# Kernel tuning notes

Hardware: AMD Instinct MI355X
Metric: run time of the kernel (lower is better)

The kernel has to match this reference:

```python
import jax, jax.numpy as jnp
import numpy as np

EMBED_DIM = 1024
NUM_HEADS = 16
HEAD_DIM = EMBED_DIM // NUM_HEADS
L, B, S = 2048, 2, 2048


def setup_inputs() -> dict:
    key = jax.random.key(0)
    k1, k2, k3, k4, k5, k6, k7 = jax.random.split(key, 7)
    query = jax.random.normal(k1, (L, B, EMBED_DIM), dtype=jnp.float32)
    kk = jax.random.normal(k2, (S, B, EMBED_DIM), dtype=jnp.float32)
    vv = jax.random.normal(k3, (S, B, EMBED_DIM), dtype=jnp.float32)
    # in_proj: Linear(E, 3E) -> weight (3E, E), bias (3E,)
    w_in = jax.random.normal(k4, (3 * EMBED_DIM, EMBED_DIM), dtype=jnp.float32) * (1.0 / np.sqrt(EMBED_DIM))
    b_in = jax.random.normal(k5, (3 * EMBED_DIM,), dtype=jnp.float32) * 0.02
    w_out = jax.random.normal(k6, (EMBED_DIM, EMBED_DIM), dtype=jnp.float32) * (1.0 / np.sqrt(EMBED_DIM))
    b_out = jax.random.normal(k7, (EMBED_DIM,), dtype=jnp.float32) * 0.02
    return {"query": query, "key": kk, "value": vv,
            "w_in": w_in, "b_in": b_in, "w_out": w_out, "b_out": b_out}


def _split_heads(x, seq_len, batch):
    # (T, B, E) -> (B, H, T, d)
    return x.reshape(seq_len, batch, NUM_HEADS, HEAD_DIM).transpose(1, 2, 0, 3)


def reference(query, key, value, w_in, b_in, w_out, b_out):
    seq_q, batch, _ = query.shape
    seq_kv = key.shape[0]
    # split fused in_proj into q/k/v projections (chunk along output rows)
    wq, wk, wv = jnp.split(w_in, 3, axis=0)
    bq, bk, bv = jnp.split(b_in, 3, axis=0)
    q = query @ wq.T + bq            # (L, B, E)
    k = key @ wk.T + bk              # (S, B, E)
    v = value @ wv.T + bv            # (S, B, E)
    q = _split_heads(q, seq_q, batch)   # (B, H, L, d)
    k = _split_heads(k, seq_kv, batch)  # (B, H, S, d)
    v = _split_heads(v, seq_kv, batch)  # (B, H, S, d)
    scale = jnp.asarray(np.sqrt(HEAD_DIM), dtype=q.dtype)
    scores = jnp.einsum('bhld,bhsd->bhls', q, k) / scale  # (B, H, L, S)
    attn = jax.nn.softmax(scores, axis=-1)
    context = jnp.einsum('bhls,bhsd->bhld', attn, v)      # (B, H, L, d)
    # (B, H, L, d) -> (L, B, E)
    context = context.transpose(2, 0, 1, 3).reshape(seq_q, batch, EMBED_DIM)
    attn_output = context @ w_out.T + b_out
    return attn_output
```

## Files before the change

### kernel.cpp

```cpp
#include <hip/hip_runtime.h>
#include <hip/hip_bf16.h>
#include <stdint.h>

#define L_SEQ 2048
#define S_SEQ 2048
#define BATCH 2
#define EMB 1024
#define NH 16
#define HD 64
#define MROWS 4096

typedef __bf16 bf16x8 __attribute__((ext_vector_type(8)));
typedef float f32x4 __attribute__((ext_vector_type(4)));
typedef __hip_bfloat16 bf16;

__device__ __forceinline__ f32x4 mfma16(bf16x8 a, bf16x8 b, f32x4 c) {
    return __builtin_amdgcn_mfma_f32_16x16x32_bf16(a, b, c, 0, 0, 0);
}

__device__ __forceinline__ void gll16(const bf16* g, bf16* l) {
    __builtin_amdgcn_global_load_lds(
        (const __attribute__((address_space(1))) void*)g,
        (__attribute__((address_space(3))) void*)l, 16, 0, 0);
}

__device__ __forceinline__ bf16x8 ld8_cvt(const float* p) {
    const float4 a = *reinterpret_cast<const float4*>(p);
    const float4 b = *reinterpret_cast<const float4*>(p + 4);
    union { bf16x8 v; bf16 h[8]; } u;
    u.h[0] = __float2bfloat16(a.x); u.h[1] = __float2bfloat16(a.y);
    u.h[2] = __float2bfloat16(a.z); u.h[3] = __float2bfloat16(a.w);
    u.h[4] = __float2bfloat16(b.x); u.h[5] = __float2bfloat16(b.y);
    u.h[6] = __float2bfloat16(b.z); u.h[7] = __float2bfloat16(b.w);
    return u.v;
}

__device__ __forceinline__ uint32_t packbf2(float a, float b) {
    const uint32_t ra = __float_as_uint(a) + 0x8000u;
    const uint32_t rb = __float_as_uint(b) + 0x8000u;
    return __builtin_amdgcn_perm(rb, ra, 0x07060302u);
}

__device__ __forceinline__ bf16x8 pfrag(const uint32_t* pk0, const uint32_t* pk1, int sk) {
    auto t0 = __builtin_amdgcn_permlane32_swap(pk0[2 * sk], pk0[2 * sk + 1], false, false);
    auto a02 = __builtin_amdgcn_permlane16_swap(t0[0], t0[1], false, false);
    auto t1 = __builtin_amdgcn_permlane32_swap(pk1[2 * sk], pk1[2 * sk + 1], false, false);
    auto a13 = __builtin_amdgcn_permlane16_swap(t1[0], t1[1], false, false);
    union { uint32_t u[4]; bf16x8 v; } pf;
    pf.u[0] = a02[0]; pf.u[1] = a13[0]; pf.u[2] = a02[1]; pf.u[3] = a13[1];
    return pf.v;
}

__global__ __launch_bounds__(256) void cvt_kernel(
    const float* __restrict__ w_in, const float* __restrict__ w_out,
    const float* __restrict__ q_in, const float* __restrict__ k_in,
    const float* __restrict__ v_in,
    bf16* __restrict__ wib, bf16* __restrict__ wob,
    bf16* __restrict__ Xq, bf16* __restrict__ Xk, bf16* __restrict__ Xv)
{
    const size_t i = ((size_t)blockIdx.x * 256 + threadIdx.x) * 8;
    const size_t o1 = (size_t)3 * EMB * EMB;
    const size_t o2 = o1 + (size_t)EMB * EMB;
    const size_t o3 = o2 + (size_t)MROWS * EMB;
    const size_t o4 = o3 + (size_t)MROWS * EMB;
    const float* src; bf16* dst; size_t j;
    if      (i < o1) { src = w_in;  dst = wib; j = i; }
    else if (i < o2) { src = w_out; dst = wob; j = i - o1; }
    else if (i < o3) { src = q_in;  dst = Xq;  j = i - o2; }
    else if (i < o4) { src = k_in;  dst = Xk;  j = i - o3; }
    else             { src = v_in;  dst = Xv;  j = i - o4; }
    *reinterpret_cast<bf16x8*>(dst + j) = ld8_cvt(src + j);
}

__global__ __launch_bounds__(256) void qkv_gemm(
    const bf16* __restrict__ Xq, const bf16* __restrict__ Xk,
    const bf16* __restrict__ Xv, const bf16* __restrict__ wib,
    const float* __restrict__ b_in,
    bf16* __restrict__ Qh, bf16* __restrict__ Kh, bf16* __restrict__ Vt)
{
    __shared__ alignas(16) bf16 lds_a[2][128 * 32];
    __shared__ alignas(16) bf16 lds_b[2][128 * 32];

    const int tid  = threadIdx.x;
    const int lane = tid & 63;
    const int wv   = tid >> 6;
    const int quad = lane >> 4;
    const int lx   = lane & 15;

    const int m0  = blockIdx.x * 128;
    const int n0g = blockIdx.y * 128;
    const int chunk = n0g >> 10;
    const bf16* Aop = (chunk == 0) ? Xq : (chunk == 1) ? Xk : Xv;

    const int wm = (wv >> 1) * 64;
    const int wn = (wv & 1) * 64;

    const int gr = 16 * wv + (lane >> 2);
    const int gc = (lane & 3) * 8;
    const bf16* gA = Aop + (size_t)(m0 + gr) * EMB + gc;
    const bf16* gB = wib + (size_t)(n0g + gr) * EMB + gc;
    bf16* lA = &lds_a[0][wv * 512];
    bf16* lB = &lds_b[0][wv * 512];
    const int BUF = 128 * 32;

    f32x4 acc[4][4];
#pragma unroll
    for (int i = 0; i < 4; i++)
#pragma unroll
        for (int j = 0; j < 4; j++) acc[i][j] = (f32x4){0.f, 0.f, 0.f, 0.f};

    gll16(gA, lA);
    gll16(gA + 64 * EMB, lA + 2048);
    gll16(gB, lB);
    gll16(gB + 64 * EMB, lB + 2048);
    __syncthreads();

    int cur = 0;
    for (int kt = 0; kt < EMB; kt += 32) {
        if (kt + 32 < EMB) {
            const int nx = cur ^ 1;
            gll16(gA + kt + 32, lA + nx * BUF);
            gll16(gA + 64 * EMB + kt + 32, lA + nx * BUF + 2048);
            gll16(gB + kt + 32, lB + nx * BUF);
            gll16(gB + 64 * EMB + kt + 32, lB + nx * BUF + 2048);
        }

        bf16x8 af[4], bfv[4];
        const int ka = quad * 8;
        const bf16* pa = &lds_a[cur][0];
        const bf16* pb = &lds_b[cur][0];
#pragma unroll
        for (int sm = 0; sm < 4; sm++)
            af[sm] = *reinterpret_cast<const bf16x8*>(pa + (wm + sm * 16 + lx) * 32 + ka);
#pragma unroll
        for (int sn = 0; sn < 4; sn++)
            bfv[sn] = *reinterpret_cast<const bf16x8*>(pb + (wn + sn * 16 + lx) * 32 + ka);
#pragma unroll
        for (int sm = 0; sm < 4; sm++)
#pragma unroll
            for (int sn = 0; sn < 4; sn++)
                acc[sm][sn] = mfma16(af[sm], bfv[sn], acc[sm][sn]);

        if (kt + 32 < EMB) __syncthreads();
        cur ^= 1;
    }

    const float scale = (chunk == 0) ? 0.18033688011112042f : 1.0f;
    bf16* dst = (chunk == 0) ? Qh : (chunk == 1) ? Kh : Vt;
#pragma unroll
    for (int sn = 0; sn < 4; sn++) {
        const int n_g = n0g + wn + sn * 16 + lx;
        const float bias = b_in[n_g];
        const int nc = n_g & (EMB - 1);
        const int h  = nc >> 6;
        const int dd = nc & 63;
#pragma unroll
        for (int sm = 0; sm < 4; sm++) {
#pragma unroll
            for (int r = 0; r < 4; r++) {
                const int m_g = m0 + wm + sm * 16 + quad * 4 + r;
                const int t = m_g >> 1;
                const int b = m_g & 1;
                const int bhidx = b * NH + h;
                const float v = (acc[sm][sn][r] + bias) * scale;
                const size_t off = (chunk == 2)
                    ? ((size_t)bhidx * HD + dd) * S_SEQ + t
                    : ((size_t)bhidx * S_SEQ + t) * HD + dd;
                dst[off] = __float2bfloat16(v);
            }
        }
    }
}

__global__ __launch_bounds__(256, 2) void attn_kernel(
    const bf16* __restrict__ Qh, const bf16* __restrict__ Kh,
    const bf16* __restrict__ Vt, bf16* __restrict__ ctx)
{
    __shared__ alignas(16) bf16 k_lds[2][128 * 64];
    __shared__ alignas(16) bf16 v_lds[2][64 * 128];

    const int tid  = threadIdx.x;
    const int lane = tid & 63;
    const int wv   = tid >> 6;
    const int quad = lane >> 4;
    const int lx   = lane & 15;
    const int lx7  = lane & 7;

    const int bh = blockIdx.y;
    const int l0 = blockIdx.x * 128;
    const int q0 = wv * 32;

    const bf16* Kbase = Kh + (size_t)bh * S_SEQ * HD;
    const bf16* Vbase = Vt + (size_t)bh * HD * S_SEQ;

    const bf16* qrow = Qh + ((size_t)bh * L_SEQ + l0 + q0 + lx) * HD + quad * 8;
    const bf16x8 qa0 = *reinterpret_cast<const bf16x8*>(qrow);
    const bf16x8 qa1 = *reinterpret_cast<const bf16x8*>(qrow + 32);
    const bf16x8 qb0 = *reinterpret_cast<const bf16x8*>(qrow + 16 * HD);
    const bf16x8 qb1 = *reinterpret_cast<const bf16x8*>(qrow + 16 * HD + 32);

    f32x4 rva = (f32x4){0.f, 0.f, 0.f, 0.f};
    f32x4 rvb = (f32x4){0.f, 0.f, 0.f, 0.f};
    f32x4 acca[4], accb[4];
#pragma unroll
    for (int sn = 0; sn < 4; sn++) {
        acca[sn] = (f32x4){0.f, 0.f, 0.f, 0.f};
        accb[sn] = (f32x4){0.f, 0.f, 0.f, 0.f};
    }

    const int kr = tid >> 3;
    const int kj = tid & 7;
    const bf16* gK = Kbase + (size_t)kr * HD + ((kj ^ (kr & 7)) << 3);
    const int vd = tid >> 4;
    const int vj = tid & 15;
    const bf16* gV = Vbase + (size_t)vd * S_SEQ + ((vj ^ (vd & 7)) << 3);

    bf16* kdst[2] = { &k_lds[0][wv * 512], &k_lds[1][wv * 512] };
    bf16* vdst[2] = { &v_lds[0][wv * 512], &v_lds[1][wv * 512] };

#pragma unroll
    for (int i = 0; i < 4; i++) {
        gll16(gK + (size_t)(i * 32) * HD, kdst[0] + i * 2048);
        gll16(gV + (size_t)(i * 16) * S_SEQ, vdst[0] + i * 2048);
    }

    int cur = 0;
    for (int s0 = 0; s0 < S_SEQ; s0 += 128) {
        __syncthreads();

        if (s0 + 128 < S_SEQ) {
            bf16* kd = kdst[cur ^ 1];
            bf16* vdp = vdst[cur ^ 1];
#pragma unroll
            for (int i = 0; i < 4; i++) {
                gll16(gK + (size_t)(s0 + 128 + i * 32) * HD, kd + i * 2048);
                gll16(gV + (size_t)(i * 16) * S_SEQ + s0 + 128, vdp + i * 2048);
            }
        }
        const bf16* kb = &k_lds[cur][0];
        const bf16* vb = &v_lds[cur][0];

        f32x4 sa[8], sb[8];
#pragma unroll
        for (int c = 0; c < 8; c++) {
            const bf16* krp = kb + (c * 16 + lx) * 64;
            bf16x8 kf0 = *reinterpret_cast<const bf16x8*>(krp + ((quad ^ lx7) << 3));
            bf16x8 kf1 = *reinterpret_cast<const bf16x8*>(krp + (((quad + 4) ^ lx7) << 3));
            f32x4 t0 = (f32x4){0.f, 0.f, 0.f, 0.f};
            t0 = mfma16(kf0, qa0, t0);
            t0 = mfma16(kf1, qa1, t0);
            sa[c] = t0;
            f32x4 t1 = (f32x4){0.f, 0.f, 0.f, 0.f};
            t1 = mfma16(kf0, qb0, t1);
            t1 = mfma16(kf1, qb1, t1);
            sb[c] = t1;
        }

        uint32_t pka0[8], pka1[8], pkb0[8], pkb1[8];
#pragma unroll
        for (int c = 0; c < 8; c++) {
#pragma unroll
            for (int r = 0; r < 4; r++) sa[c][r] = __builtin_amdgcn_exp2f(sa[c][r]);
            rva += sa[c];
            pka0[c] = packbf2(sa[c][0], sa[c][1]);
            pka1[c] = packbf2(sa[c][2], sa[c][3]);
        }
#pragma unroll
        for (int c = 0; c < 8; c++) {
#pragma unroll
            for (int r = 0; r < 4; r++) sb[c][r] = __builtin_amdgcn_exp2f(sb[c][r]);
            rvb += sb[c];
            pkb0[c] = packbf2(sb[c][0], sb[c][1]);
            pkb1[c] = packbf2(sb[c][2], sb[c][3]);
        }

#pragma unroll
        for (int sk = 0; sk < 4; sk++) {
            const bf16x8 pfa = pfrag(pka0, pka1, sk);
            const bf16x8 pfb = pfrag(pkb0, pkb1, sk);
#pragma unroll
            for (int sn = 0; sn < 4; sn++) {
                const bf16x8 vf = *reinterpret_cast<const bf16x8*>(
                    vb + (sn * 16 + lx) * 128 + (((sk * 4 + quad) ^ lx7) << 3));
                acca[sn] = mfma16(pfa, vf, acca[sn]);
                accb[sn] = mfma16(pfb, vf, accb[sn]);
            }
        }
        cur ^= 1;
    }

    float la = (rva[0] + rva[1]) + (rva[2] + rva[3]);
    la += __shfl_xor(la, 16);
    la += __shfl_xor(la, 32);
    float lbs = (rvb[0] + rvb[1]) + (rvb[2] + rvb[3]);
    lbs += __shfl_xor(lbs, 16);
    lbs += __shfl_xor(lbs, 32);

    const int b = bh >> 4;
    const int h = bh & 15;
#pragma unroll
    for (int r = 0; r < 4; r++) {
        const float lra = __shfl(la, quad * 20 + r);
        const float lrb = __shfl(lbs, quad * 20 + r);
        const float inva = 1.f / lra;
        const float invb = 1.f / lrb;
        const int lA = l0 + q0 + quad * 4 + r;
        const int lB = lA + 16;
#pragma unroll
        for (int sn = 0; sn < 4; sn++) {
            const int dd = sn * 16 + lx;
            ctx[(size_t)(lA * BATCH + b) * EMB + h * HD + dd] =
                __float2bfloat16(acca[sn][r] * inva);
            ctx[(size_t)(lB * BATCH + b) * EMB + h * HD + dd] =
                __float2bfloat16(accb[sn][r] * invb);
        }
    }
}

__global__ __launch_bounds__(256) void out_gemm(
    const bf16* __restrict__ ctx, const bf16* __restrict__ wob,
    const float* __restrict__ b_out, float* __restrict__ out)
{
    __shared__ alignas(16) bf16 lds_a[2][64 * 32];
    __shared__ alignas(16) bf16 lds_b[2][128 * 32];

    const int tid  = threadIdx.x;
    const int lane = tid & 63;
    const int wv   = tid >> 6;
    const int quad = lane >> 4;
    const int lx   = lane & 15;

    const int m0 = blockIdx.x * 64;
    const int n0 = blockIdx.y * 128;

    const int wm = (wv >> 1) * 32;
    const int wn = (wv & 1) * 64;

    const int gr = 16 * wv + (lane >> 2);
    const int gc = (lane & 3) * 8;
    const bf16* gA = ctx + (size_t)(m0 + gr) * EMB + gc;
    const bf16* gB = wob + (size_t)(n0 + gr) * EMB + gc;
    bf16* lA = &lds_a[0][wv * 512];
    bf16* lB = &lds_b[0][wv * 512];
    const int BUFA = 64 * 32;
    const int BUFB = 128 * 32;

    f32x4 acc[2][4];
#pragma unroll
    for (int i = 0; i < 2; i++)
#pragma unroll
        for (int j = 0; j < 4; j++) acc[i][j] = (f32x4){0.f, 0.f, 0.f, 0.f};

    gll16(gA, lA);
    gll16(gB, lB);
    gll16(gB + 64 * EMB, lB + 2048);
    __syncthreads();

    int cur = 0;
    for (int kt = 0; kt < EMB; kt += 32) {
        if (kt + 32 < EMB) {
            const int nx = cur ^ 1;
            gll16(gA + kt + 32, lA + nx * BUFA);
            gll16(gB + kt + 32, lB + nx * BUFB);
            gll16(gB + 64 * EMB + kt + 32, lB + nx * BUFB + 2048);
        }

        bf16x8 af[2], bfv[4];
        const int ka = quad * 8;
        const bf16* pa = &lds_a[cur][0];
        const bf16* pb = &lds_b[cur][0];
#pragma unroll
        for (int sm = 0; sm < 2; sm++)
            af[sm] = *reinterpret_cast<const bf16x8*>(pa + (wm + sm * 16 + lx) * 32 + ka);
#pragma unroll
        for (int sn = 0; sn < 4; sn++)
            bfv[sn] = *reinterpret_cast<const bf16x8*>(pb + (wn + sn * 16 + lx) * 32 + ka);
#pragma unroll
        for (int sm = 0; sm < 2; sm++)
#pragma unroll
            for (int sn = 0; sn < 4; sn++)
                acc[sm][sn] = mfma16(af[sm], bfv[sn], acc[sm][sn]);

        if (kt + 32 < EMB) __syncthreads();
        cur ^= 1;
    }

#pragma unroll
    for (int sn = 0; sn < 4; sn++) {
        const int n_g = n0 + wn + sn * 16 + lx;
        const float bias = b_out[n_g];
#pragma unroll
        for (int sm = 0; sm < 2; sm++) {
#pragma unroll
            for (int r = 0; r < 4; r++) {
                const int m_g = m0 + wm + sm * 16 + quad * 4 + r;
                out[(size_t)m_g * EMB + n_g] = acc[sm][sn][r] + bias;
            }
        }
    }
}

extern "C" void kernel_launch(void* const* d_in, const int* in_sizes, int n_in,
                              void* d_out, int out_size, void* d_ws, size_t ws_size,
                              hipStream_t stream)
{
    const float* query = (const float*)d_in[0];
    const float* key_  = (const float*)d_in[1];
    const float* value = (const float*)d_in[2];
    const float* w_in  = (const float*)d_in[3];
    const float* b_in  = (const float*)d_in[4];
    const float* w_out = (const float*)d_in[5];
    const float* b_out = (const float*)d_in[6];
    float* out = (float*)d_out;

    const size_t seg = (size_t)MROWS * EMB;
    bf16* wib = (bf16*)d_ws;
    bf16* wob = wib + (size_t)3 * EMB * EMB;
    bf16* Xq  = wob + (size_t)EMB * EMB;
    bf16* Xk  = Xq + seg;
    bf16* Xv  = Xk + seg;
    bf16* Qh  = Xv + seg;
    bf16* Kh  = Qh + seg;
    bf16* Vt  = Kh + seg;
    bf16* ctx = Xq;

    cvt_kernel<<<8192, 256, 0, stream>>>(w_in, w_out, query, key_, value,
                                         wib, wob, Xq, Xk, Xv);
    qkv_gemm<<<dim3(32, 24), 256, 0, stream>>>(Xq, Xk, Xv, wib, b_in, Qh, Kh, Vt);
    attn_kernel<<<dim3(16, 32), 256, 0, stream>>>(Qh, Kh, Vt, ctx);
    out_gemm<<<dim3(64, 8), 256, 0, stream>>>(ctx, wob, b_out, out);
}
```

Baseline: 217.2 us.

## Fuse fp32-to-bf16 activation conversion into QKV GEMM tile loads

Removes the separate conversion of query/key/value to bf16 and instead streams fp32 activation tiles directly into LDS via global_load_lds with an XOR swizzle. Conversion to bf16 happens while building MFMA fragments. This drops a full read+write pass over 3x4096x1024 activations, but doubles the A-tile LDS footprint and global traffic per GEMM tile (each tile is re-read by 8 column blocks in fp32), and adds packing ALU work in the inner loop.

```diff
diff --git a/kernel.cpp b/kernel.cpp
--- a/kernel.cpp
+++ b/kernel.cpp
@@ -19,6 +19,11 @@
 }
 
 __device__ __forceinline__ void gll16(const bf16* g, bf16* l) {
+    __builtin_amdgcn_global_load_lds(
+        (const __attribute__((address_space(1))) void*)g,
+        (__attribute__((address_space(3))) void*)l, 16, 0, 0);
+}
+__device__ __forceinline__ void gllf(const float* g, float* l) {
     __builtin_amdgcn_global_load_lds(
         (const __attribute__((address_space(1))) void*)g,
         (__attribute__((address_space(3))) void*)l, 16, 0, 0);
@@ -41,6 +46,13 @@
     return __builtin_amdgcn_perm(rb, ra, 0x07060302u);
 }
 
+__device__ __forceinline__ bf16x8 pack8(float4 lo, float4 hi) {
+    union { uint32_t u[4]; bf16x8 v; } t;
+    t.u[0] = packbf2(lo.x, lo.y); t.u[1] = packbf2(lo.z, lo.w);
+    t.u[2] = packbf2(hi.x, hi.y); t.u[3] = packbf2(hi.z, hi.w);
+    return t.v;
+}
+
 __device__ __forceinline__ bf16x8 pfrag(const uint32_t* pk0, const uint32_t* pk1, int sk) {
     auto t0 = __builtin_amdgcn_permlane32_swap(pk0[2 * sk], pk0[2 * sk + 1], false, false);
     auto a02 = __builtin_amdgcn_permlane16_swap(t0[0], t0[1], false, false);
@@ -53,55 +65,45 @@
 
 __global__ __launch_bounds__(256) void cvt_kernel(
     const float* __restrict__ w_in, const float* __restrict__ w_out,
-    const float* __restrict__ q_in, const float* __restrict__ k_in,
-    const float* __restrict__ v_in,
-    bf16* __restrict__ wib, bf16* __restrict__ wob,
-    bf16* __restrict__ Xq, bf16* __restrict__ Xk, bf16* __restrict__ Xv)
+    bf16* __restrict__ wib, bf16* __restrict__ wob)
 {
     const size_t i = ((size_t)blockIdx.x * 256 + threadIdx.x) * 8;
     const size_t o1 = (size_t)3 * EMB * EMB;
-    const size_t o2 = o1 + (size_t)EMB * EMB;
-    const size_t o3 = o2 + (size_t)MROWS * EMB;
-    const size_t o4 = o3 + (size_t)MROWS * EMB;
-    const float* src; bf16* dst; size_t j;
-    if      (i < o1) { src = w_in;  dst = wib; j = i; }
-    else if (i < o2) { src = w_out; dst = wob; j = i - o1; }
-    else if (i < o3) { src = q_in;  dst = Xq;  j = i - o2; }
-    else if (i < o4) { src = k_in;  dst = Xk;  j = i - o3; }
-    else             { src = v_in;  dst = Xv;  j = i - o4; }
-    *reinterpret_cast<bf16x8*>(dst + j) = ld8_cvt(src + j);
+    if (i < o1) *reinterpret_cast<bf16x8*>(wib + i) = ld8_cvt(w_in + i);
+    else        *reinterpret_cast<bf16x8*>(wob + (i - o1)) = ld8_cvt(w_out + (i - o1));
 }
 
 __global__ __launch_bounds__(256) void qkv_gemm(
-    const bf16* __restrict__ Xq, const bf16* __restrict__ Xk,
-    const bf16* __restrict__ Xv, const bf16* __restrict__ wib,
+    const float* __restrict__ Xq, const float* __restrict__ Xk,
+    const float* __restrict__ Xv, const bf16* __restrict__ wib,
     const float* __restrict__ b_in,
     bf16* __restrict__ Qh, bf16* __restrict__ Kh, bf16* __restrict__ Vt)
 {
-    __shared__ alignas(16) bf16 lds_a[2][128 * 32];
-    __shared__ alignas(16) bf16 lds_b[2][128 * 32];
+    __shared__ alignas(16) float lds_a[2][128 * 32];
+    __shared__ alignas(16) bf16  lds_b[2][128 * 32];
 
     const int tid  = threadIdx.x;
     const int lane = tid & 63;
     const int wv   = tid >> 6;
     const int quad = lane >> 4;
     const int lx   = lane & 15;
+    const int lx7  = lane & 7;
 
     const int m0  = blockIdx.x * 128;
     const int n0g = blockIdx.y * 128;
     const int chunk = n0g >> 10;
-    const bf16* Aop = (chunk == 0) ? Xq : (chunk == 1) ? Xk : Xv;
+    const float* Aop = (chunk == 0) ? Xq : (chunk == 1) ? Xk : Xv;
 
     const int wm = (wv >> 1) * 64;
     const int wn = (wv & 1) * 64;
 
+    const int arow = tid >> 3;
+    const int acs  = ((tid & 7) ^ (arow & 7)) * 4;
+    const float* gA = Aop + (size_t)(m0 + arow) * EMB + acs;
+
     const int gr = 16 * wv + (lane >> 2);
     const int gc = (lane & 3) * 8;
-    const bf16* gA = Aop + (size_t)(m0 + gr) * EMB + gc;
     const bf16* gB = wib + (size_t)(n0g + gr) * EMB + gc;
-    bf16* lA = &lds_a[0][wv * 512];
-    bf16* lB = &lds_b[0][wv * 512];
-    const int BUF = 128 * 32;
 
     f32x4 acc[4][4];
 #pragma unroll
@@ -109,29 +111,35 @@
 #pragma unroll
         for (int j = 0; j < 4; j++) acc[i][j] = (f32x4){0.f, 0.f, 0.f, 0.f};
 
-    gll16(gA, lA);
-    gll16(gA + 64 * EMB, lA + 2048);
-    gll16(gB, lB);
-    gll16(gB + 64 * EMB, lB + 2048);
+#pragma unroll
+    for (int i = 0; i < 4; i++)
+        gllf(gA + (size_t)(i * 32) * EMB, &lds_a[0][i * 1024 + wv * 256]);
+    gll16(gB, &lds_b[0][wv * 512]);
+    gll16(gB + 64 * EMB, &lds_b[0][wv * 512 + 2048]);
     __syncthreads();
 
     int cur = 0;
     for (int kt = 0; kt < EMB; kt += 32) {
         if (kt + 32 < EMB) {
             const int nx = cur ^ 1;
-            gll16(gA + kt + 32, lA + nx * BUF);
-            gll16(gA + 64 * EMB + kt + 32, lA + nx * BUF + 2048);
-            gll16(gB + kt + 32, lB + nx * BUF);
-            gll16(gB + 64 * EMB + kt + 32, lB + nx * BUF + 2048);
+#pragma unroll
+            for (int i = 0; i < 4; i++)
+                gllf(gA + (size_t)(i * 32) * EMB + kt + 32, &lds_a[nx][i * 1024 + wv * 256]);
+            gll16(gB + kt + 32, &lds_b[nx][wv * 512]);
+            gll16(gB + 64 * EMB + kt + 32, &lds_b[nx][wv * 512 + 2048]);
         }
 
         bf16x8 af[4], bfv[4];
         const int ka = quad * 8;
-        const bf16* pa = &lds_a[cur][0];
-        const bf16* pb = &lds_b[cur][0];
-#pragma unroll
-        for (int sm = 0; sm < 4; sm++)
-            af[sm] = *reinterpret_cast<const bf16x8*>(pa + (wm + sm * 16 + lx) * 32 + ka);
+        const float* pa = &lds_a[cur][0];
+        const bf16*  pb = &lds_b[cur][0];
+#pragma unroll
+        for (int sm = 0; sm < 4; sm++) {
+            const float* pr = pa + (wm + sm * 16 + lx) * 32;
+            const float4 lo = *reinterpret_cast<const float4*>(pr + (((2 * quad)     ^ lx7) * 4));
+            const float4 hi = *reinterpret_cast<const float4*>(pr + (((2 * quad + 1) ^ lx7) * 4));
+            af[sm] = pack8(lo, hi);
+        }
 #pragma unroll
         for (int sn = 0; sn < 4; sn++)
             bfv[sn] = *reinterpret_cast<const bf16x8*>(pb + (wn + sn * 16 + lx) * 32 + ka);
@@ -416,17 +424,13 @@
     const size_t seg = (size_t)MROWS * EMB;
     bf16* wib = (bf16*)d_ws;
     bf16* wob = wib + (size_t)3 * EMB * EMB;
-    bf16* Xq  = wob + (size_t)EMB * EMB;
-    bf16* Xk  = Xq + seg;
-    bf16* Xv  = Xk + seg;
-    bf16* Qh  = Xv + seg;
+    bf16* Qh  = wob + (size_t)EMB * EMB;
     bf16* Kh  = Qh + seg;
     bf16* Vt  = Kh + seg;
-    bf16* ctx = Xq;
-
-    cvt_kernel<<<8192, 256, 0, stream>>>(w_in, w_out, query, key_, value,
-                                         wib, wob, Xq, Xk, Xv);
-    qkv_gemm<<<dim3(32, 24), 256, 0, stream>>>(Xq, Xk, Xv, wib, b_in, Qh, Kh, Vt);
+    bf16* ctx = Vt + seg;
+
+    cvt_kernel<<<2048, 256, 0, stream>>>(w_in, w_out, wib, wob);
+    qkv_gemm<<<dim3(32, 24), 256, 0, stream>>>(query, key_, value, wib, b_in, Qh, Kh, Vt);
     attn_kernel<<<dim3(16, 32), 256, 0, stream>>>(Qh, Kh, Vt, ctx);
     out_gemm<<<dim3(64, 8), 256, 0, stream>>>(ctx, wob, b_out, out);
 }
```

Measured after the change: 266.3 us. +22.6%, slower.
